# Performance work log

Hardware: AMD Instinct MI355X
Metric: run time of the kernel (lower is better)

Reference implementation:

```python
import jax, jax.numpy as jnp
import numpy as np


def _patch_size(w):
    # mirrors PatchLoss size selection (static shape -> Python branch is fine)
    if w == 512:
        return 64
    elif 256 <= w < 512:
        return 32
    raise ValueError('error size')


def setup_inputs() -> dict:
    key = jax.random.key(0)
    k1, k2 = jax.random.split(key)
    shape = (1, 3, 32, 512, 512)  # (b=1, c, t, h, w)
    x = jax.random.normal(k1, shape, dtype=jnp.float32)
    x_r = jax.random.normal(k2, shape, dtype=jnp.float32)
    return {"x": x, "x_r": x_r}


def reference(x, x_r):
    _, c, t, h, w = x.shape
    size = _patch_size(w)
    tc, hc, wc = 1, size // 2, size // 2
    # L = |(x+1)/2 - (x_r+1)/2| ; original detaches before pooling
    L = jnp.abs((x + 1.0) / 2.0 - (x_r + 1.0) / 2.0)
    D = jax.lax.stop_gradient(L)[0]  # (c, t, h, w), batch squeezed
    # patch means over (c, hc, wc) for each frame (tc=1) and spatial block
    nh, nw = h // hc, w // wc
    P = D.reshape(c, t, nh, hc, nw, wc).mean(axis=(0, 3, 5))  # (t, nh, nw)
    # max over spatial patches; original init max_patch=0.0, so clamp at 0
    max_patches = jnp.maximum(P.max(axis=(1, 2)), 0.0)  # (t,)
    return jnp.log(max_patches.mean())
```

## Files before the change

### kernel.cpp

```cpp
#include <hip/hip_runtime.h>
#include <math.h>


typedef float vf4 __attribute__((ext_vector_type(4)));

__global__ __launch_bounds__(256) void patch_sum_kernel(
    const float* __restrict__ x, const float* __restrict__ xr,
    float* __restrict__ part) {
  const int b   = blockIdx.x;
  const int tid = threadIdx.x;
  const size_t base4 = (size_t)b * 3 * 2048;
  const vf4* __restrict__ a4 = (const vf4*)x  + base4;
  const vf4* __restrict__ c4 = (const vf4*)xr + base4;

  float acc0 = 0.f, acc1 = 0.f, acc2 = 0.f;
#pragma unroll
  for (int i = 0; i < 8; ++i) {
    int o = i * 256 + tid;
    vf4 a0 = __builtin_nontemporal_load(&a4[o]);
    vf4 c0 = __builtin_nontemporal_load(&c4[o]);
    vf4 a1 = __builtin_nontemporal_load(&a4[2048 + o]);
    vf4 c1 = __builtin_nontemporal_load(&c4[2048 + o]);
    vf4 a2 = __builtin_nontemporal_load(&a4[4096 + o]);
    vf4 c2 = __builtin_nontemporal_load(&c4[4096 + o]);
    acc0 += fabsf(a0.x - c0.x) + fabsf(a0.y - c0.y)
          + fabsf(a0.z - c0.z) + fabsf(a0.w - c0.w);
    acc1 += fabsf(a1.x - c1.x) + fabsf(a1.y - c1.y)
          + fabsf(a1.z - c1.z) + fabsf(a1.w - c1.w);
    acc2 += fabsf(a2.x - c2.x) + fabsf(a2.y - c2.y)
          + fabsf(a2.z - c2.z) + fabsf(a2.w - c2.w);
  }

#pragma unroll
  for (int o = 4; o > 0; o >>= 1) {
    acc0 += __shfl_down(acc0, o, 8);
    acc1 += __shfl_down(acc1, o, 8);
    acc2 += __shfl_down(acc2, o, 8);
  }
  __shared__ float s[3][32];
  if ((tid & 7) == 0) {
    int m = tid >> 3;
    s[0][m] = acc0;
    s[1][m] = acc1;
    s[2][m] = acc2;
  }
  __syncthreads();
  if (tid < 48) {
    int k = tid >> 4;
    int bin = tid & 15;
    part[(size_t)(b * 3 + k) * 16 + bin] = s[k][bin] + s[k][bin + 16];
  }
}

__global__ __launch_bounds__(1024) void finalize_kernel(
    const float* __restrict__ part, float* __restrict__ out) {
  const int tid = threadIdx.x;
  const int t = tid >> 5;
  const int j = tid & 31;
  float m = -1e30f;
#pragma unroll
  for (int k = 0; k < 8; ++k) {
    int p = t * 256 + j + 32 * k;
    int ph = (p >> 4) & 15;
    int pw = p & 15;
    float v = 0.f;
#pragma unroll
    for (int ch = 0; ch < 3; ++ch) {
#pragma unroll
      for (int half = 0; half < 2; ++half) {
        int idx = ((ch << 10) + (t << 5) + (ph << 1) + half) * 16 + pw;
        v += part[idx];
      }
    }
    m = fmaxf(m, v);
  }
#pragma unroll
  for (int o = 16; o > 0; o >>= 1) m = fmaxf(m, __shfl_down(m, o, 32));
  __shared__ float s[32];
  if (j == 0) s[t] = fmaxf(m * (0.5f / 3072.0f), 0.f);
  __syncthreads();
  if (tid < 32) {
    float v = s[tid];
#pragma unroll
    for (int o = 16; o > 0; o >>= 1) v += __shfl_down(v, o, 32);
    if (tid == 0) out[0] = logf(v * (1.0f / 32.0f));
  }
}

extern "C" void kernel_launch(void* const* d_in, const int* in_sizes, int n_in,
                              void* d_out, int out_size, void* d_ws, size_t ws_size,
                              hipStream_t stream) {
  const float* x  = (const float*)d_in[0];
  const float* xr = (const float*)d_in[1];
  float* part = (float*)d_ws;
  float* out  = (float*)d_out;

  patch_sum_kernel<<<1024, 256, 0, stream>>>(x, xr, part);
  finalize_kernel<<<1, 1024, 0, stream>>>(part, out);
}
```

Baseline: 194.8 us.

## Fuse patch sum and finalize into one kernel with last-block reduction

Result: slower. 227.1 us (+16.6%).

```diff
diff --git a/kernel.cpp b/kernel.cpp
--- a/kernel.cpp
+++ b/kernel.cpp
@@ -4,86 +4,79 @@
 
 typedef float vf4 __attribute__((ext_vector_type(4)));
 
-__global__ __launch_bounds__(256) void patch_sum_kernel(
+__device__ int g_count = 0;
+
+__global__ __launch_bounds__(512, 4) void patch_loss_kernel(
     const float* __restrict__ x, const float* __restrict__ xr,
-    float* __restrict__ part) {
+    float* __restrict__ bm, float* __restrict__ out) {
   const int b   = blockIdx.x;
   const int tid = threadIdx.x;
-  const size_t base4 = (size_t)b * 3 * 2048;
-  const vf4* __restrict__ a4 = (const vf4*)x  + base4;
-  const vf4* __restrict__ c4 = (const vf4*)xr + base4;
+  const int t  = b >> 4;
+  const int ph = b & 15;
+  const size_t s0 = ((size_t)(t)      << 16) + ((size_t)ph << 12);
+  const size_t s1 = ((size_t)(32 + t) << 16) + ((size_t)ph << 12);
+  const size_t s2 = ((size_t)(64 + t) << 16) + ((size_t)ph << 12);
+  const vf4* __restrict__ a4 = (const vf4*)x;
+  const vf4* __restrict__ c4 = (const vf4*)xr;
 
   float acc0 = 0.f, acc1 = 0.f, acc2 = 0.f;
 #pragma unroll
   for (int i = 0; i < 8; ++i) {
-    int o = i * 256 + tid;
-    vf4 a0 = __builtin_nontemporal_load(&a4[o]);
-    vf4 c0 = __builtin_nontemporal_load(&c4[o]);
-    vf4 a1 = __builtin_nontemporal_load(&a4[2048 + o]);
-    vf4 c1 = __builtin_nontemporal_load(&c4[2048 + o]);
-    vf4 a2 = __builtin_nontemporal_load(&a4[4096 + o]);
-    vf4 c2 = __builtin_nontemporal_load(&c4[4096 + o]);
-    acc0 += fabsf(a0.x - c0.x) + fabsf(a0.y - c0.y)
-          + fabsf(a0.z - c0.z) + fabsf(a0.w - c0.w);
-    acc1 += fabsf(a1.x - c1.x) + fabsf(a1.y - c1.y)
-          + fabsf(a1.z - c1.z) + fabsf(a1.w - c1.w);
-    acc2 += fabsf(a2.x - c2.x) + fabsf(a2.y - c2.y)
-          + fabsf(a2.z - c2.z) + fabsf(a2.w - c2.w);
+    int o = i * 512 + tid;
+    vf4 A0 = __builtin_nontemporal_load(&a4[s0 + o]);
+    vf4 C0 = __builtin_nontemporal_load(&c4[s0 + o]);
+    vf4 A1 = __builtin_nontemporal_load(&a4[s1 + o]);
+    vf4 C1 = __builtin_nontemporal_load(&c4[s1 + o]);
+    vf4 A2 = __builtin_nontemporal_load(&a4[s2 + o]);
+    vf4 C2 = __builtin_nontemporal_load(&c4[s2 + o]);
+    acc0 += fabsf(A0.x - C0.x) + fabsf(A0.y - C0.y)
+          + fabsf(A0.z - C0.z) + fabsf(A0.w - C0.w);
+    acc1 += fabsf(A1.x - C1.x) + fabsf(A1.y - C1.y)
+          + fabsf(A1.z - C1.z) + fabsf(A1.w - C1.w);
+    acc2 += fabsf(A2.x - C2.x) + fabsf(A2.y - C2.y)
+          + fabsf(A2.z - C2.z) + fabsf(A2.w - C2.w);
+  }
+  float acc = acc0 + acc1 + acc2;
+#pragma unroll
+  for (int o = 4; o > 0; o >>= 1) acc += __shfl_down(acc, o, 8);
+
+  __shared__ float sp[16][4];
+  if ((tid & 7) == 0) sp[(tid >> 3) & 15][tid >> 7] = acc;
+  __syncthreads();
+
+  float bmax = 0.f;
+  if (tid < 16) {
+    float v = sp[tid][0] + sp[tid][1] + sp[tid][2] + sp[tid][3];
+#pragma unroll
+    for (int o = 8; o > 0; o >>= 1) v = fmaxf(v, __shfl_down(v, o, 16));
+    bmax = v;
   }
 
-#pragma unroll
-  for (int o = 4; o > 0; o >>= 1) {
-    acc0 += __shfl_down(acc0, o, 8);
-    acc1 += __shfl_down(acc1, o, 8);
-    acc2 += __shfl_down(acc2, o, 8);
-  }
-  __shared__ float s[3][32];
-  if ((tid & 7) == 0) {
-    int m = tid >> 3;
-    s[0][m] = acc0;
-    s[1][m] = acc1;
-    s[2][m] = acc2;
+  __shared__ int is_last;
+  if (tid == 0) {
+    __hip_atomic_store(&bm[b], bmax * (0.5f / 3072.0f),
+                       __ATOMIC_RELAXED, __HIP_MEMORY_SCOPE_AGENT);
+    __threadfence();
+    int old = __hip_atomic_fetch_add(&g_count, 1, __ATOMIC_ACQ_REL,
+                                     __HIP_MEMORY_SCOPE_AGENT);
+    is_last = ((old & 511) == 511);
   }
   __syncthreads();
-  if (tid < 48) {
-    int k = tid >> 4;
-    int bin = tid & 15;
-    part[(size_t)(b * 3 + k) * 16 + bin] = s[k][bin] + s[k][bin + 16];
-  }
-}
+  if (!is_last) return;
 
-__global__ __launch_bounds__(1024) void finalize_kernel(
-    const float* __restrict__ part, float* __restrict__ out) {
-  const int tid = threadIdx.x;
-  const int t = tid >> 5;
-  const int j = tid & 31;
-  float m = -1e30f;
+  __threadfence();
+  float v = __hip_atomic_load(&bm[tid], __ATOMIC_RELAXED,
+                              __HIP_MEMORY_SCOPE_AGENT);
 #pragma unroll
-  for (int k = 0; k < 8; ++k) {
-    int p = t * 256 + j + 32 * k;
-    int ph = (p >> 4) & 15;
-    int pw = p & 15;
-    float v = 0.f;
-#pragma unroll
-    for (int ch = 0; ch < 3; ++ch) {
-#pragma unroll
-      for (int half = 0; half < 2; ++half) {
-        int idx = ((ch << 10) + (t << 5) + (ph << 1) + half) * 16 + pw;
-        v += part[idx];
-      }
-    }
-    m = fmaxf(m, v);
-  }
-#pragma unroll
-  for (int o = 16; o > 0; o >>= 1) m = fmaxf(m, __shfl_down(m, o, 32));
-  __shared__ float s[32];
-  if (j == 0) s[t] = fmaxf(m * (0.5f / 3072.0f), 0.f);
+  for (int o = 8; o > 0; o >>= 1) v = fmaxf(v, __shfl_down(v, o, 16));
+  __shared__ float st[32];
+  if ((tid & 15) == 0) st[tid >> 4] = fmaxf(v, 0.f);
   __syncthreads();
   if (tid < 32) {
-    float v = s[tid];
+    float s = st[tid];
 #pragma unroll
-    for (int o = 16; o > 0; o >>= 1) v += __shfl_down(v, o, 32);
-    if (tid == 0) out[0] = logf(v * (1.0f / 32.0f));
+    for (int o = 16; o > 0; o >>= 1) s += __shfl_down(s, o, 32);
+    if (tid == 0) out[0] = logf(s * (1.0f / 32.0f));
   }
 }
 
@@ -92,9 +85,8 @@
                               hipStream_t stream) {
   const float* x  = (const float*)d_in[0];
   const float* xr = (const float*)d_in[1];
-  float* part = (float*)d_ws;
-  float* out  = (float*)d_out;
+  float* bm  = (float*)d_ws;
+  float* out = (float*)d_out;
 
-  patch_sum_kernel<<<1024, 256, 0, stream>>>(x, xr, part);
-  finalize_kernel<<<1, 1024, 0, stream>>>(part, out);
+  patch_loss_kernel<<<512, 512, 0, stream>>>(x, xr, bm, out);
 }
```

## Stream inputs through double-buffered LDS via async global_load_lds pipeline

Applied to the files above, without the earlier changes.

Result: slower. 216.4 us (+11.1%).

```diff
diff --git a/kernel.cpp b/kernel.cpp
--- a/kernel.cpp
+++ b/kernel.cpp
@@ -4,51 +4,72 @@
 
 typedef float vf4 __attribute__((ext_vector_type(4)));
 
-__global__ __launch_bounds__(256) void patch_sum_kernel(
+#define AS1(p) ((const __attribute__((address_space(1))) void*)(p))
+#define AS3(p) ((__attribute__((address_space(3))) void*)(p))
+
+__global__ __launch_bounds__(256, 4) void patch_sum_kernel(
     const float* __restrict__ x, const float* __restrict__ xr,
     float* __restrict__ part) {
+  __shared__ vf4 lA[2][512];
+  __shared__ vf4 lC[2][512];
   const int b   = blockIdx.x;
   const int tid = threadIdx.x;
-  const size_t base4 = (size_t)b * 3 * 2048;
-  const vf4* __restrict__ a4 = (const vf4*)x  + base4;
-  const vf4* __restrict__ c4 = (const vf4*)xr + base4;
+  const size_t base = (size_t)b * 98304;
+  const char* __restrict__ ga = (const char*)x  + base + (size_t)tid * 16;
+  const char* __restrict__ gc = (const char*)xr + base + (size_t)tid * 16;
+  const int wv = (tid >> 6) << 6;
 
-  float acc0 = 0.f, acc1 = 0.f, acc2 = 0.f;
+  auto stage = [&](int s, int p) {
+    const size_t off = (size_t)s * 8192;
+    __builtin_amdgcn_global_load_lds(AS1(ga + off),        AS3(&lA[p][wv]),        16, 0, 0);
+    __builtin_amdgcn_global_load_lds(AS1(ga + off + 4096), AS3(&lA[p][256 + wv]),  16, 0, 0);
+    __builtin_amdgcn_global_load_lds(AS1(gc + off),        AS3(&lC[p][wv]),        16, 0, 0);
+    __builtin_amdgcn_global_load_lds(AS1(gc + off + 4096), AS3(&lC[p][256 + wv]),  16, 0, 0);
+  };
+
+  stage(0, 0);
+  stage(1, 1);
+  float acc[3] = {0.f, 0.f, 0.f};
+
 #pragma unroll
-  for (int i = 0; i < 8; ++i) {
-    int o = i * 256 + tid;
-    vf4 a0 = __builtin_nontemporal_load(&a4[o]);
-    vf4 c0 = __builtin_nontemporal_load(&c4[o]);
-    vf4 a1 = __builtin_nontemporal_load(&a4[2048 + o]);
-    vf4 c1 = __builtin_nontemporal_load(&c4[2048 + o]);
-    vf4 a2 = __builtin_nontemporal_load(&a4[4096 + o]);
-    vf4 c2 = __builtin_nontemporal_load(&c4[4096 + o]);
-    acc0 += fabsf(a0.x - c0.x) + fabsf(a0.y - c0.y)
-          + fabsf(a0.z - c0.z) + fabsf(a0.w - c0.w);
-    acc1 += fabsf(a1.x - c1.x) + fabsf(a1.y - c1.y)
-          + fabsf(a1.z - c1.z) + fabsf(a1.w - c1.w);
-    acc2 += fabsf(a2.x - c2.x) + fabsf(a2.y - c2.y)
-          + fabsf(a2.z - c2.z) + fabsf(a2.w - c2.w);
+  for (int s = 0; s < 12; ++s) {
+    const int p = s & 1;
+    if (s < 11) {
+      asm volatile("s_waitcnt vmcnt(4)" ::: "memory");
+    } else {
+      asm volatile("s_waitcnt vmcnt(0)" ::: "memory");
+    }
+    __builtin_amdgcn_s_barrier();
+    vf4 A0 = lA[p][tid];       vf4 C0 = lC[p][tid];
+    vf4 A1 = lA[p][256 + tid]; vf4 C1 = lC[p][256 + tid];
+    float d = fabsf(A0.x - C0.x) + fabsf(A0.y - C0.y)
+            + fabsf(A0.z - C0.z) + fabsf(A0.w - C0.w)
+            + fabsf(A1.x - C1.x) + fabsf(A1.y - C1.y)
+            + fabsf(A1.z - C1.z) + fabsf(A1.w - C1.w);
+    acc[s >> 2] += d;
+    __builtin_amdgcn_s_barrier();
+    if (s + 2 < 12) stage(s + 2, p);
   }
 
+  float acc0 = acc[0], acc1 = acc[1], acc2 = acc[2];
 #pragma unroll
   for (int o = 4; o > 0; o >>= 1) {
     acc0 += __shfl_down(acc0, o, 8);
     acc1 += __shfl_down(acc1, o, 8);
     acc2 += __shfl_down(acc2, o, 8);
   }
-  __shared__ float s[3][32];
+  __shared__ float sred[3][32];
   if ((tid & 7) == 0) {
     int m = tid >> 3;
-    s[0][m] = acc0;
-    s[1][m] = acc1;
-    s[2][m] = acc2;
+    sred[0][m] = acc0;
+    sred[1][m] = acc1;
+    sred[2][m] = acc2;
   }
   __syncthreads();
   if (tid < 48) {
     int k = tid >> 4;
     int bin = tid & 15;
-    part[(size_t)(b * 3 + k) * 16 + bin] = s[k][bin] + s[k][bin + 16];
+    part[(size_t)(b * 3 + k) * 16 + bin] = sred[k][bin] + sred[k][bin + 16];
   }
 }
 
```
